# Performance work log

Hardware: AMD Instinct MI355X
Metric: run time of the kernel (lower is better)

Reference implementation:

```python
import jax, jax.numpy as jnp
import numpy as np

B, H, W, C = 8, 64, 64, 768
NH, HD = 12, 64          # num_heads, head_dim
WS = 16                  # window size
SCALE = HD ** -0.5


def setup_inputs() -> dict:
    key = jax.random.key(0)
    ks = jax.random.split(key, 6)
    x = jax.random.normal(ks[0], (B, H * W, C), dtype=jnp.float32)
    w_qkv = jax.random.normal(ks[1], (3 * C, C), dtype=jnp.float32) * 0.02
    w_out = jax.random.normal(ks[2], (C, C), dtype=jnp.float32) * 0.02
    b_out = jnp.zeros((C,), dtype=jnp.float32)
    rel_pos_h = jax.random.normal(ks[3], (2 * WS - 1, HD), dtype=jnp.float32) * 0.02
    rel_pos_w = jax.random.normal(ks[4], (2 * WS - 1, HD), dtype=jnp.float32) * 0.02
    return {"x": x, "w_qkv": w_qkv, "w_out": w_out, "b_out": b_out,
            "rel_pos_h": rel_pos_h, "rel_pos_w": rel_pos_w}


def reference(x, w_qkv, w_out, b_out, rel_pos_h, rel_pos_w):
    nh_w, nw_w = H // WS, W // WS
    xw = x.reshape(B, nh_w, WS, nw_w, WS, C).transpose(0, 1, 3, 2, 4, 5)
    Bw = B * nh_w * nw_w
    t = WS * WS
    xw = xw.reshape(Bw, t, C)

    # ---- qkv projection (no bias) and rearrange 'b t (qkv l d) -> qkv b l t d'
    qkv = (xw @ w_qkv.T).reshape(Bw, t, 3, NH, HD).transpose(2, 0, 3, 1, 4)
    q, k, v = qkv[0], qkv[1], qkv[2]        # each (Bw, NH, t, HD)

    # ---- scaled attention scores
    att = jnp.einsum('bhxd,bhyd->bhxy', q, k) * SCALE   # (Bw, NH, t, t)

    # ---- decomposed relative position bias (SAM/MViT style, q_size == k_size == WS)
    idx = jnp.arange(WS)[:, None] - jnp.arange(WS)[None, :] + (WS - 1)  # (WS, WS)
    Rh = rel_pos_h[idx]                      # (WS, WS, HD)
    Rw = rel_pos_w[idx]                      # (WS, WS, HD)
    rq = q.reshape(Bw * NH, WS, WS, HD)
    rel_h = jnp.einsum('bhwc,hkc->bhwk', rq, Rh)   # (Bw*NH, WS, WS, WS)
    rel_w = jnp.einsum('bhwc,wkc->bhwk', rq, Rw)
    att = (att.reshape(Bw * NH, WS, WS, WS, WS)
           + rel_h[:, :, :, :, None]
           + rel_w[:, :, :, None, :]).reshape(Bw, NH, t, t)

    # ---- softmax + AV
    att = jax.nn.softmax(att, axis=-1)
    o = jnp.einsum('bhxy,bhyd->bhxd', att, v)          # (Bw, NH, t, HD)
    o = o.transpose(0, 2, 1, 3).reshape(Bw, t, C)      # 'b h l d -> b l (h d)'

    # ---- output projection
    o = o @ w_out.T + b_out

    # ---- window unpartition back to (B, H*W, C)
    o = o.reshape(B, nh_w, nw_w, WS, WS, C).transpose(0, 1, 3, 2, 4, 5)
    return o.reshape(B, H * W, C)
```

## Files before the change

kernel.cpp:

```cpp
#include <hip/hip_runtime.h>

typedef __attribute__((ext_vector_type(8))) short bf16x8;
typedef __attribute__((ext_vector_type(4))) float f32x4;
typedef unsigned short u16;

__device__ __forceinline__ u16 f2bf(float f) {
  union { float f; unsigned u; } v; v.f = f;
  unsigned r = v.u + 0x7fffu + ((v.u >> 16) & 1u);
  return (u16)(r >> 16);
}
__device__ __forceinline__ float bf2f(u16 u) {
  union { unsigned u; float f; } v; v.u = ((unsigned)u) << 16;
  return v.f;
}
__device__ __forceinline__ void gload16(const void* g, void* l) {
  __builtin_amdgcn_global_load_lds((const __attribute__((address_space(1))) void*)g,
                                   (__attribute__((address_space(3))) void*)l, 16, 0, 0);
}

#define PH_BAR __builtin_amdgcn_s_barrier()
#define LGKM0  asm volatile("s_waitcnt lgkmcnt(0)" ::: "memory")
#define VM6    asm volatile("s_waitcnt vmcnt(6)" ::: "memory")
#define VM0    asm volatile("s_waitcnt vmcnt(0)" ::: "memory")

__global__ void sab_cvt_kernel(const float* __restrict__ src, u16* __restrict__ dst, int n4) {
  int i = blockIdx.x * blockDim.x + threadIdx.x;
  if (i >= n4) return;
  float4 f = reinterpret_cast<const float4*>(src)[i];
  ushort4 o; o.x = f2bf(f.x); o.y = f2bf(f.y); o.z = f2bf(f.z); o.w = f2bf(f.w);
  reinterpret_cast<ushort4*>(dst)[i] = o;
}

__global__ void sab_xw_kernel(const float* __restrict__ x, u16* __restrict__ xw) {
  const int total = 32768 * 192;
  for (int idx = blockIdx.x * 256 + threadIdx.x; idx < total; idx += gridDim.x * 256) {
    const int r = idx / 192, c = idx - r * 192;
    const int w = r >> 8, tt = r & 255;
    const long xrow = (long)(w >> 4) * 4096 + (((w >> 2) & 3) * 16 + (tt >> 4)) * 64 + (w & 3) * 16 + (tt & 15);
    float4 f = reinterpret_cast<const float4*>(x)[xrow * 192 + c];
    ushort4 o; o.x = f2bf(f.x); o.y = f2bf(f.y); o.z = f2bf(f.z); o.w = f2bf(f.w);
    reinterpret_cast<ushort4*>(xw)[idx] = o;
  }
}

template<int EPI>
__global__ __launch_bounds__(512, 2)
void sab_gemm8_kernel(const u16* __restrict__ A, const u16* __restrict__ Bt,
                      u16* __restrict__ outB, u16* __restrict__ vTp,
                      float* __restrict__ outF, const float* __restrict__ bias,
                      const int K)
{
  __shared__ __align__(16) u16 lds[2][2][2][8192];
  const int tid = threadIdx.x;
  const int lane = tid & 63, wid = tid >> 6;
  const int wr = wid >> 2, wc = wid & 3;
  const int lr = lane & 15, lg = lane >> 4;

  const int NY = gridDim.y;
  const int bid0 = blockIdx.y * gridDim.x + blockIdx.x;
  const int xcd = bid0 & 7, local = bid0 >> 3;
  const long m0 = (long)(xcd * 16 + local / NY) * 256;
  const long n0 = (long)(local % NY) * 256;

  const int swz = ((lane & 7) ^ (lane >> 3)) << 3;
  const u16* Agl = A  + (m0 + wid * 8 + (lane >> 3)) * (long)K + swz;
  const u16* Bgl = Bt + (n0 + wid * 8 + (lane >> 3)) * (long)K + swz;

  f32x4 acc[8][4];
#pragma unroll
  for (int a = 0; a < 8; ++a)
#pragma unroll
    for (int b = 0; b < 4; ++b) acc[a][b] = (f32x4){0.f, 0.f, 0.f, 0.f};

  auto stage = [&](int buf, int mat, int half, int rb, int kt) {
    const u16* g = (mat ? Bgl : Agl) + (half * 128 + rb) * (long)K + kt;
    gload16(g, &lds[buf][mat][half][(rb + wid * 8) * 64]);
  };
  auto rdA4 = [&](int buf, int q, bf16x8 (&out)[4][2]) {
#pragma unroll
    for (int m2 = 0; m2 < 4; ++m2)
#pragma unroll
      for (int kc = 0; kc < 2; ++kc)
        out[m2][kc] = *reinterpret_cast<const bf16x8*>(
          &lds[buf][0][wr][(q * 64 + m2 * 16 + lr) * 64 + ((kc * 32 + lg * 8) ^ ((lr & 7) << 3))]);
  };
  auto rdB2 = [&](int buf, int q, bf16x8 (&out)[2][2]) {
#pragma unroll
    for (int n2 = 0; n2 < 2; ++n2)
#pragma unroll
      for (int kc = 0; kc < 2; ++kc)
        out[n2][kc] = *reinterpret_cast<const bf16x8*>(
          &lds[buf][1][wc >> 1][((wc & 1) * 64 + q * 32 + n2 * 16 + lr) * 64 + ((kc * 32 + lg * 8) ^ ((lr & 7) << 3))]);
  };
  auto mma16 = [&](bf16x8 (&a)[4][2], bf16x8 (&b)[2][2], int mq, int nq) {
    __builtin_amdgcn_s_setprio(1);
#pragma unroll
    for (int kc = 0; kc < 2; ++kc)
#pragma unroll
      for (int m2 = 0; m2 < 4; ++m2)
#pragma unroll
        for (int n2 = 0; n2 < 2; ++n2)
          acc[mq * 4 + m2][nq * 2 + n2] = __builtin_amdgcn_mfma_f32_16x16x32_bf16(
              a[m2][kc], b[n2][kc], acc[mq * 4 + m2][nq * 2 + n2], 0, 0, 0);
    __builtin_amdgcn_s_setprio(0);
  };

  stage(0,0,0,0,0);  stage(0,0,1,0,0);  stage(0,1,0,0,0);  stage(0,1,1,0,0);
  stage(0,1,0,64,0); stage(0,1,1,64,0); stage(0,0,0,64,0); stage(0,0,1,64,0);
  stage(1,0,0,0,64); stage(1,0,1,0,64); stage(1,1,0,0,64); stage(1,1,1,0,64);
  stage(1,1,0,64,64); stage(1,1,1,64,64);
  VM6; PH_BAR;

  bf16x8 af[4][2], b0[2][2], b1[2][2];

  for (int kt = 0; kt < K; kt += 128) {
    const int k2 = kt + 128, k3 = kt + 192;
    const bool s2 = k2 < K, s3 = k3 < K;
    rdA4(0, 0, af); rdB2(0, 0, b0);
    stage(1,0,0,64, kt + 64); stage(1,0,1,64, kt + 64);
    PH_BAR; LGKM0; mma16(af, b0, 0, 0); PH_BAR;
    rdB2(0, 1, b1);
    if (s2) { stage(0,0,0,0, k2); stage(0,0,1,0, k2); }
    PH_BAR; LGKM0; mma16(af, b1, 0, 1); PH_BAR;
    rdA4(0, 1, af);
    if (s2) { stage(0,1,0,0, k2); stage(0,1,1,0, k2); }
    PH_BAR; LGKM0; mma16(af, b0, 1, 0); PH_BAR;
    if (s2) { stage(0,1,0,64, k2); stage(0,1,1,64, k2); }
    PH_BAR; mma16(af, b1, 1, 1); VM6; PH_BAR;
    rdA4(1, 0, af); rdB2(1, 0, b0);
    if (s2) { stage(0,0,0,64, k2); stage(0,0,1,64, k2); }
    PH_BAR; LGKM0; mma16(af, b0, 0, 0); PH_BAR;
    rdB2(1, 1, b1);
    if (s3) { stage(1,0,0,0, k3); stage(1,0,1,0, k3); }
    PH_BAR; LGKM0; mma16(af, b1, 0, 1); PH_BAR;
    rdA4(1, 1, af);
    if (s3) { stage(1,1,0,0, k3); stage(1,1,1,0, k3); }
    PH_BAR; LGKM0; mma16(af, b0, 1, 0); PH_BAR;
    if (s3) { stage(1,1,0,64, k3); stage(1,1,1,64, k3); }
    PH_BAR; mma16(af, b1, 1, 1); VM6; PH_BAR;
  }

  VM0;
  __syncthreads();
  u16* cl = &lds[0][0][0][0];

  if (EPI == 0) {
    if (n0 < 1536) {
#pragma unroll
      for (int mt = 0; mt < 8; ++mt)
#pragma unroll
        for (int nt = 0; nt < 4; ++nt) {
          const int col = wc * 64 + nt * 16 + lr;
          const int row0 = wr * 128 + mt * 16 + lg * 4;
#pragma unroll
          for (int r = 0; r < 4; ++r)
            cl[(row0 + r) * 256 + col] = f2bf(acc[mt][nt][r]);
        }
      __syncthreads();
#pragma unroll
      for (int s = 0; s < 16; ++s) {
        const int c = s * 512 + tid;
        const int row = c >> 5, ch = c & 31;
        *reinterpret_cast<bf16x8*>(&outB[(m0 + row) * 1536 + n0 + ch * 8]) =
            *reinterpret_cast<const bf16x8*>(&cl[row * 256 + ch * 8]);
      }
    } else {
#pragma unroll
      for (int mt = 0; mt < 8; ++mt)
#pragma unroll
        for (int nt = 0; nt < 4; ++nt) {
          const int col = wc * 64 + nt * 16 + lr;
          const int row0 = wr * 128 + mt * 16 + lg * 4;
          ushort4 o;
          o.x = f2bf(acc[mt][nt][0]); o.y = f2bf(acc[mt][nt][1]);
          o.z = f2bf(acc[mt][nt][2]); o.w = f2bf(acc[mt][nt][3]);
          *reinterpret_cast<ushort4*>(&cl[col * 256 + row0]) = o;
        }
      __syncthreads();
#pragma unroll
      for (int s = 0; s < 16; ++s) {
        const int c = s * 512 + tid;
        const int d = c >> 5, ch = c & 31;
        *reinterpret_cast<bf16x8*>(&vTp[(n0 - 1536 + d) * 32768L + m0 + ch * 8]) =
            *reinterpret_cast<const bf16x8*>(&cl[d * 256 + ch * 8]);
      }
    }
  } else {
#pragma unroll
    for (int mt = 0; mt < 8; ++mt)
#pragma unroll
      for (int nt = 0; nt < 4; ++nt) {
        const long col = n0 + wc * 64 + nt * 16 + lr;
        const float bv = bias[col];
        const long row0 = m0 + wr * 128 + mt * 16 + lg * 4;
#pragma unroll
        for (int r = 0; r < 4; ++r) {
          const int rr = (int)(row0 + r);
          const int w = rr >> 8, tt = rr & 255;
          const long xrow = (long)(w >> 4) * 4096 + (((w >> 2) & 3) * 16 + (tt >> 4)) * 64 + (w & 3) * 16 + (tt & 15);
          outF[xrow * 768 + col] = acc[mt][nt][r] + bv;
        }
      }
  }
}

__global__ __launch_bounds__(256, 2)
void sab_attn_kernel(const u16* __restrict__ qk, const u16* __restrict__ vT,
                     const float* __restrict__ rph, const float* __restrict__ rpw,
                     u16* __restrict__ oatt)
{
  __shared__ __align__(16) u16 relh_s[256 * 16];
  __shared__ __align__(16) u16 relw_s[256 * 16];
  __shared__ __align__(16) u16 Sbuf[4][16 * 72];

  const int blk0 = blockIdx.x;
  const int blk = (blk0 & 7) * 192 + (blk0 >> 3);
  const int w = blk / 12, h = blk % 12;
  const long qbase = (long)w * 256;
  const int tid = threadIdx.x, lane = tid & 63, wid = tid >> 6;
  const int lr = lane & 15, lg = lane >> 4;

  const u16* Qp = qk + (long)h * 64;
  const u16* Kp = qk + 768 + (long)h * 64;
  const u16* Vt = vT + (long)h * 64 * 32768 + w * 256;

#pragma unroll
  for (int ii = 0; ii < 4; ++ii) {
    const int i = wid * 4 + ii;
    f32x4 acc = (f32x4){0.f, 0.f, 0.f, 0.f};
#pragma unroll
    for (int kc = 0; kc < 2; ++kc) {
      bf16x8 a = *reinterpret_cast<const bf16x8*>(&Qp[(qbase + i * 16 + lr) * 1536 + kc * 32 + lg * 8]);
      const float* bp = rph + (i - lr + 15) * 64 + kc * 32 + lg * 8;
      bf16x8 b;
#pragma unroll
      for (int e = 0; e < 8; ++e) b[e] = (short)f2bf(bp[e]);
      acc = __builtin_amdgcn_mfma_f32_16x16x32_bf16(a, b, acc, 0, 0, 0);
    }
#pragma unroll
    for (int r = 0; r < 4; ++r)
      relh_s[(i * 16 + lg * 4 + r) * 16 + lr] = f2bf(acc[r]);
  }
#pragma unroll
  for (int jj = 0; jj < 4; ++jj) {
    const int j = wid * 4 + jj;
    f32x4 acc = (f32x4){0.f, 0.f, 0.f, 0.f};
#pragma unroll
    for (int kc = 0; kc < 2; ++kc) {
      bf16x8 a = *reinterpret_cast<const bf16x8*>(&Qp[(qbase + lr * 16 + j) * 1536 + kc * 32 + lg * 8]);
      const float* bp = rpw + (j - lr + 15) * 64 + kc * 32 + lg * 8;
      bf16x8 b;
#pragma unroll
      for (int e = 0; e < 8; ++e) b[e] = (short)f2bf(bp[e]);
      acc = __builtin_amdgcn_mfma_f32_16x16x32_bf16(a, b, acc, 0, 0, 0);
    }
#pragma unroll
    for (int r = 0; r < 4; ++r)
      relw_s[((lg * 4 + r) * 16 + j) * 16 + lr] = f2bf(acc[r]);
  }
  __syncthreads();

  bf16x8 qa[4][2];
#pragma unroll
  for (int mt = 0; mt < 4; ++mt)
#pragma unroll
    for (int kc = 0; kc < 2; ++kc)
      qa[mt][kc] = *reinterpret_cast<const bf16x8*>(&Qp[(qbase + wid * 64 + mt * 16 + lr) * 1536 + kc * 32 + lg * 8]);

  float rw[4][4];
#pragma unroll
  for (int mt = 0; mt < 4; ++mt)
#pragma unroll
    for (int r = 0; r < 4; ++r)
      rw[mt][r] = bf2f(relw_s[(wid * 64 + mt * 16 + lg * 4 + r) * 16 + lr]);

  float mrun[4][4], lrun[4][4];
  f32x4 oacc[4][4];
#pragma unroll
  for (int mt = 0; mt < 4; ++mt)
#pragma unroll
    for (int r = 0; r < 4; ++r) { mrun[mt][r] = -1e30f; lrun[mt][r] = 0.f; }
#pragma unroll
  for (int mt = 0; mt < 4; ++mt)
#pragma unroll
    for (int nt = 0; nt < 4; ++nt) oacc[mt][nt] = (f32x4){0.f, 0.f, 0.f, 0.f};

  u16* sb = &Sbuf[wid][0];

  for (int kb = 0; kb < 4; ++kb) {
    bf16x8 kf[4][2], vf[4][2];
#pragma unroll
    for (int nt = 0; nt < 4; ++nt)
#pragma unroll
      for (int kc = 0; kc < 2; ++kc) {
        kf[nt][kc] = *reinterpret_cast<const bf16x8*>(&Kp[(qbase + kb * 64 + nt * 16 + lr) * 1536 + kc * 32 + lg * 8]);
        vf[nt][kc] = *reinterpret_cast<const bf16x8*>(&Vt[(nt * 16 + lr) * 32768L + kb * 64 + kc * 32 + lg * 8]);
      }

#pragma unroll
    for (int mt = 0; mt < 4; ++mt) {
      f32x4 sn[4];
#pragma unroll
      for (int nt = 0; nt < 4; ++nt) {
        f32x4 t = (f32x4){0.f, 0.f, 0.f, 0.f};
#pragma unroll
        for (int kc = 0; kc < 2; ++kc)
          t = __builtin_amdgcn_mfma_f32_16x16x32_bf16(qa[mt][kc], kf[nt][kc], t, 0, 0, 0);
        sn[nt] = t;
      }
#pragma unroll
      for (int r = 0; r < 4; ++r) {
        const int x = wid * 64 + mt * 16 + lg * 4 + r;
        float sv[4];
#pragma unroll
        for (int nt = 0; nt < 4; ++nt)
          sv[nt] = sn[nt][r] * 0.125f + bf2f(relh_s[x * 16 + kb * 4 + nt]) + rw[mt][r];
        float rmax = fmaxf(fmaxf(sv[0], sv[1]), fmaxf(sv[2], sv[3]));
        rmax = fmaxf(rmax, __shfl_xor(rmax, 1));
        rmax = fmaxf(rmax, __shfl_xor(rmax, 2));
        rmax = fmaxf(rmax, __shfl_xor(rmax, 4));
        rmax = fmaxf(rmax, __shfl_xor(rmax, 8));
        const float mnew = fmaxf(mrun[mt][r], rmax);
        const float sf = __expf(mrun[mt][r] - mnew);
        mrun[mt][r] = mnew;
        float rsum = 0.f;
#pragma unroll
        for (int nt = 0; nt < 4; ++nt) { const float p = __expf(sv[nt] - mnew); sv[nt] = p; rsum += p; }
        lrun[mt][r] = lrun[mt][r] * sf + rsum;
#pragma unroll
        for (int nt = 0; nt < 4; ++nt) oacc[mt][nt][r] *= sf;
        const int rowl = lg * 4 + r;
#pragma unroll
        for (int nt = 0; nt < 4; ++nt) sb[rowl * 72 + nt * 16 + lr] = f2bf(sv[nt]);
      }
#pragma unroll
      for (int kc = 0; kc < 2; ++kc) {
        bf16x8 pa = *reinterpret_cast<const bf16x8*>(&sb[lr * 72 + kc * 32 + lg * 8]);
#pragma unroll
        for (int nt = 0; nt < 4; ++nt)
          oacc[mt][nt] = __builtin_amdgcn_mfma_f32_16x16x32_bf16(pa, vf[nt][kc], oacc[mt][nt], 0, 0, 0);
      }
    }
  }

#pragma unroll
  for (int mt = 0; mt < 4; ++mt)
#pragma unroll
    for (int r = 0; r < 4; ++r) {
      float lt = lrun[mt][r];
      lt += __shfl_xor(lt, 1);
      lt += __shfl_xor(lt, 2);
      lt += __shfl_xor(lt, 4);
      lt += __shfl_xor(lt, 8);
      const float inv = 1.f / lt;
      const long row = qbase + wid * 64 + mt * 16 + lg * 4 + r;
#pragma unroll
      for (int nt = 0; nt < 4; ++nt)
        oatt[row * 768 + h * 64 + nt * 16 + lr] = f2bf(oacc[mt][nt][r] * inv);
    }
}

extern "C" void kernel_launch(void* const* d_in, const int* in_sizes, int n_in,
                              void* d_out, int out_size, void* d_ws, size_t ws_size,
                              hipStream_t stream) {
  (void)in_sizes; (void)n_in; (void)out_size; (void)ws_size;
  const float* x     = (const float*)d_in[0];
  const float* w_qkv = (const float*)d_in[1];
  const float* w_out = (const float*)d_in[2];
  const float* b_out = (const float*)d_in[3];
  const float* rph   = (const float*)d_in[4];
  const float* rpw   = (const float*)d_in[5];
  float* out = (float*)d_out;

  char* ws = (char*)d_ws;
  u16* qk    = (u16*)ws;
  u16* vT    = (u16*)(ws + 100663296L);
  u16* xw    = (u16*)(ws + 150994944L);
  u16* wqkvb = (u16*)(ws + 201326592L);
  u16* woutb = (u16*)(ws + 204865536L);
  u16* oatt  = xw;

  sab_cvt_kernel<<<dim3(1728), dim3(256), 0, stream>>>(w_qkv, wqkvb, 442368);
  sab_cvt_kernel<<<dim3(576), dim3(256), 0, stream>>>(w_out, woutb, 147456);
  sab_xw_kernel<<<dim3(6144), dim3(256), 0, stream>>>(x, xw);
  sab_gemm8_kernel<0><<<dim3(128, 9), dim3(512), 0, stream>>>(xw, wqkvb, qk, vT, nullptr, nullptr, 768);
  sab_attn_kernel<<<dim3(1536), dim3(256), 0, stream>>>(qk, vT, rph, rpw, oatt);
  sab_gemm8_kernel<1><<<dim3(128, 3), dim3(512), 0, stream>>>(oatt, woutb, nullptr, nullptr, out, b_out, 768);
}
```

Measured before the change: 356.7 us.

## Use 16 waves per GEMM block with 2x8 warp grid and halved per-wave tiles

The 256x256-tile bf16 GEMM now runs with 1024 threads (16 waves) instead of 512, arranged 2x8 so each wave owns a 128x32 sub-tile. Staging is rebalanced so each wave issues half as many global-to-LDS loads, and the vmcnt waits change to match. The epilogues are adjusted for the narrower per-wave columns. This cuts per-wave accumulator registers and loads and adds waves for latency hiding, but each wave re-reads the A fragments from LDS with less reuse per B fragment, and fewer blocks fit per CU.

```diff
diff --git a/kernel.cpp b/kernel.cpp
--- a/kernel.cpp
+++ b/kernel.cpp
@@ -20,7 +20,7 @@
 
 #define PH_BAR __builtin_amdgcn_s_barrier()
 #define LGKM0  asm volatile("s_waitcnt lgkmcnt(0)" ::: "memory")
-#define VM6    asm volatile("s_waitcnt vmcnt(6)" ::: "memory")
+#define VM3    asm volatile("s_waitcnt vmcnt(3)" ::: "memory")
 #define VM0    asm volatile("s_waitcnt vmcnt(0)" ::: "memory")
 
 __global__ void sab_cvt_kernel(const float* __restrict__ src, u16* __restrict__ dst, int n4) {
@@ -44,7 +44,7 @@
 }
 
 template<int EPI>
-__global__ __launch_bounds__(512, 2)
+__global__ __launch_bounds__(1024)
 void sab_gemm8_kernel(const u16* __restrict__ A, const u16* __restrict__ Bt,
                       u16* __restrict__ outB, u16* __restrict__ vTp,
                       float* __restrict__ outF, const float* __restrict__ bias,
@@ -53,7 +53,7 @@
   __shared__ __align__(16) u16 lds[2][2][2][8192];
   const int tid = threadIdx.x;
   const int lane = tid & 63, wid = tid >> 6;
-  const int wr = wid >> 2, wc = wid & 3;
+  const int wr = wid >> 3, wc = wid & 7;
   const int lr = lane & 15, lg = lane >> 4;
 
   const int NY = gridDim.y;
@@ -62,19 +62,21 @@
   const long m0 = (long)(xcd * 16 + local / NY) * 256;
   const long n0 = (long)(local % NY) * 256;
 
-  const int swz = ((lane & 7) ^ (lane >> 3)) << 3;
-  const u16* Agl = A  + (m0 + wid * 8 + (lane >> 3)) * (long)K + swz;
-  const u16* Bgl = Bt + (n0 + wid * 8 + (lane >> 3)) * (long)K + swz;
-
-  f32x4 acc[8][4];
+  const int shalf = wid >> 3;
+  const int srow  = (wid & 7) * 8 + (lane >> 3);
+  const int swz   = ((lane & 7) ^ ((lane >> 3) & 7)) << 3;
+  const u16* Agl = A  + (m0 + shalf * 128 + srow) * (long)K + swz;
+  const u16* Bgl = Bt + (n0 + shalf * 128 + srow) * (long)K + swz;
+
+  f32x4 acc[8][2];
 #pragma unroll
   for (int a = 0; a < 8; ++a)
 #pragma unroll
-    for (int b = 0; b < 4; ++b) acc[a][b] = (f32x4){0.f, 0.f, 0.f, 0.f};
-
-  auto stage = [&](int buf, int mat, int half, int rb, int kt) {
-    const u16* g = (mat ? Bgl : Agl) + (half * 128 + rb) * (long)K + kt;
-    gload16(g, &lds[buf][mat][half][(rb + wid * 8) * 64]);
+    for (int b = 0; b < 2; ++b) acc[a][b] = (f32x4){0.f, 0.f, 0.f, 0.f};
+
+  auto stage = [&](int buf, int mat, int q, int kt) {
+    const u16* g = (mat ? Bgl : Agl) + (long)q * 64 * K + kt;
+    gload16(g, &lds[buf][mat][shalf][(q * 64 + (wid & 7) * 8) * 64]);
   };
   auto rdA4 = [&](int buf, int q, bf16x8 (&out)[4][2]) {
 #pragma unroll
@@ -84,60 +86,56 @@
         out[m2][kc] = *reinterpret_cast<const bf16x8*>(
           &lds[buf][0][wr][(q * 64 + m2 * 16 + lr) * 64 + ((kc * 32 + lg * 8) ^ ((lr & 7) << 3))]);
   };
-  auto rdB2 = [&](int buf, int q, bf16x8 (&out)[2][2]) {
-#pragma unroll
-    for (int n2 = 0; n2 < 2; ++n2)
-#pragma unroll
-      for (int kc = 0; kc < 2; ++kc)
-        out[n2][kc] = *reinterpret_cast<const bf16x8*>(
-          &lds[buf][1][wc >> 1][((wc & 1) * 64 + q * 32 + n2 * 16 + lr) * 64 + ((kc * 32 + lg * 8) ^ ((lr & 7) << 3))]);
+  auto rdB1 = [&](int buf, int nq, bf16x8 (&out)[2]) {
+#pragma unroll
+    for (int kc = 0; kc < 2; ++kc)
+      out[kc] = *reinterpret_cast<const bf16x8*>(
+        &lds[buf][1][wc >> 2][(((wc & 3) * 32 + nq * 16 + lr)) * 64 + ((kc * 32 + lg * 8) ^ ((lr & 7) << 3))]);
   };
-  auto mma16 = [&](bf16x8 (&a)[4][2], bf16x8 (&b)[2][2], int mq, int nq) {
+  auto mma8 = [&](bf16x8 (&a)[4][2], bf16x8 (&b)[2], int mq, int nq) {
     __builtin_amdgcn_s_setprio(1);
 #pragma unroll
     for (int kc = 0; kc < 2; ++kc)
 #pragma unroll
       for (int m2 = 0; m2 < 4; ++m2)
-#pragma unroll
-        for (int n2 = 0; n2 < 2; ++n2)
-          acc[mq * 4 + m2][nq * 2 + n2] = __builtin_amdgcn_mfma_f32_16x16x32_bf16(
-              a[m2][kc], b[n2][kc], acc[mq * 4 + m2][nq * 2 + n2], 0, 0, 0);
+        acc[mq * 4 + m2][nq] = __builtin_amdgcn_mfma_f32_16x16x32_bf16(
+            a[m2][kc], b[kc], acc[mq * 4 + m2][nq], 0, 0, 0);
     __builtin_amdgcn_s_setprio(0);
   };
 
-  stage(0,0,0,0,0);  stage(0,0,1,0,0);  stage(0,1,0,0,0);  stage(0,1,1,0,0);
-  stage(0,1,0,64,0); stage(0,1,1,64,0); stage(0,0,0,64,0); stage(0,0,1,64,0);
-  stage(1,0,0,0,64); stage(1,0,1,0,64); stage(1,1,0,0,64); stage(1,1,1,0,64);
-  stage(1,1,0,64,64); stage(1,1,1,64,64);
-  VM6; PH_BAR;
-
-  bf16x8 af[4][2], b0[2][2], b1[2][2];
+  stage(0,0,0,0); stage(0,0,1,0); stage(0,1,0,0); stage(0,1,1,0);
+  stage(1,0,0,64); stage(1,1,0,64); stage(1,1,1,64);
+  VM3; PH_BAR;
+
+  bf16x8 af[4][2], b0[2], b1[2];
 
   for (int kt = 0; kt < K; kt += 128) {
     const int k2 = kt + 128, k3 = kt + 192;
     const bool s2 = k2 < K, s3 = k3 < K;
-    rdA4(0, 0, af); rdB2(0, 0, b0);
-    stage(1,0,0,64, kt + 64); stage(1,0,1,64, kt + 64);
-    PH_BAR; LGKM0; mma16(af, b0, 0, 0); PH_BAR;
-    rdB2(0, 1, b1);
-    if (s2) { stage(0,0,0,0, k2); stage(0,0,1,0, k2); }
-    PH_BAR; LGKM0; mma16(af, b1, 0, 1); PH_BAR;
+    rdA4(0, 0, af); rdB1(0, 0, b0);
+    stage(1,0,1, kt + 64);
+    PH_BAR; LGKM0; mma8(af, b0, 0, 0); PH_BAR;
+    rdB1(0, 1, b1);
+    if (s2) stage(0,0,0, k2);
+    PH_BAR; LGKM0; mma8(af, b1, 0, 1); PH_BAR;
     rdA4(0, 1, af);
-    if (s2) { stage(0,1,0,0, k2); stage(0,1,1,0, k2); }
-    PH_BAR; LGKM0; mma16(af, b0, 1, 0); PH_BAR;
-    if (s2) { stage(0,1,0,64, k2); stage(0,1,1,64, k2); }
-    PH_BAR; mma16(af, b1, 1, 1); VM6; PH_BAR;
-    rdA4(1, 0, af); rdB2(1, 0, b0);
-    if (s2) { stage(0,0,0,64, k2); stage(0,0,1,64, k2); }
-    PH_BAR; LGKM0; mma16(af, b0, 0, 0); PH_BAR;
-    rdB2(1, 1, b1);
-    if (s3) { stage(1,0,0,0, k3); stage(1,0,1,0, k3); }
-    PH_BAR; LGKM0; mma16(af, b1, 0, 1); PH_BAR;
+    if (s2) stage(0,1,0, k2);
+    PH_BAR; LGKM0; mma8(af, b0, 1, 0); PH_BAR;
+    if (s2) stage(0,1,1, k2);
+    PH_BAR; mma8(af, b1, 1, 1);
+    if (s2) { VM3; } else { VM0; }
+    PH_BAR;
+    rdA4(1, 0, af); rdB1(1, 0, b0);
+    if (s2) stage(0,0,1, k2);
+    PH_BAR; LGKM0; mma8(af, b0, 0, 0); PH_BAR;
+    rdB1(1, 1, b1);
+    if (s3) stage(1,0,0, k3);
+    PH_BAR; LGKM0; mma8(af, b1, 0, 1); PH_BAR;
     rdA4(1, 1, af);
-    if (s3) { stage(1,1,0,0, k3); stage(1,1,1,0, k3); }
-    PH_BAR; LGKM0; mma16(af, b0, 1, 0); PH_BAR;
-    if (s3) { stage(1,1,0,64, k3); stage(1,1,1,64, k3); }
-    PH_BAR; mma16(af, b1, 1, 1); VM6; PH_BAR;
+    if (s3) stage(1,1,0, k3);
+    PH_BAR; LGKM0; mma8(af, b0, 1, 0); PH_BAR;
+    if (s3) stage(1,1,1, k3);
+    PH_BAR; mma8(af, b1, 1, 1); VM3; PH_BAR;
   }
 
   VM0;
@@ -149,8 +147,8 @@
 #pragma unroll
       for (int mt = 0; mt < 8; ++mt)
 #pragma unroll
-        for (int nt = 0; nt < 4; ++nt) {
-          const int col = wc * 64 + nt * 16 + lr;
+        for (int nt = 0; nt < 2; ++nt) {
+          const int col = wc * 32 + nt * 16 + lr;
           const int row0 = wr * 128 + mt * 16 + lg * 4;
 #pragma unroll
           for (int r = 0; r < 4; ++r)
@@ -158,8 +156,8 @@
         }
       __syncthreads();
 #pragma unroll
-      for (int s = 0; s < 16; ++s) {
-        const int c = s * 512 + tid;
+      for (int s = 0; s < 8; ++s) {
+        const int c = s * 1024 + tid;
         const int row = c >> 5, ch = c & 31;
         *reinterpret_cast<bf16x8*>(&outB[(m0 + row) * 1536 + n0 + ch * 8]) =
             *reinterpret_cast<const bf16x8*>(&cl[row * 256 + ch * 8]);
@@ -168,8 +166,8 @@
 #pragma unroll
       for (int mt = 0; mt < 8; ++mt)
 #pragma unroll
-        for (int nt = 0; nt < 4; ++nt) {
-          const int col = wc * 64 + nt * 16 + lr;
+        for (int nt = 0; nt < 2; ++nt) {
+          const int col = wc * 32 + nt * 16 + lr;
           const int row0 = wr * 128 + mt * 16 + lg * 4;
           ushort4 o;
           o.x = f2bf(acc[mt][nt][0]); o.y = f2bf(acc[mt][nt][1]);
@@ -178,8 +176,8 @@
         }
       __syncthreads();
 #pragma unroll
-      for (int s = 0; s < 16; ++s) {
-        const int c = s * 512 + tid;
+      for (int s = 0; s < 8; ++s) {
+        const int c = s * 1024 + tid;
         const int d = c >> 5, ch = c & 31;
         *reinterpret_cast<bf16x8*>(&vTp[(n0 - 1536 + d) * 32768L + m0 + ch * 8]) =
             *reinterpret_cast<const bf16x8*>(&cl[d * 256 + ch * 8]);
@@ -189,8 +187,8 @@
 #pragma unroll
     for (int mt = 0; mt < 8; ++mt)
 #pragma unroll
-      for (int nt = 0; nt < 4; ++nt) {
-        const long col = n0 + wc * 64 + nt * 16 + lr;
+      for (int nt = 0; nt < 2; ++nt) {
+        const long col = n0 + wc * 32 + nt * 16 + lr;
         const float bv = bias[col];
         const long row0 = m0 + wr * 128 + mt * 16 + lg * 4;
 #pragma unroll
@@ -383,7 +381,7 @@
   sab_cvt_kernel<<<dim3(1728), dim3(256), 0, stream>>>(w_qkv, wqkvb, 442368);
   sab_cvt_kernel<<<dim3(576), dim3(256), 0, stream>>>(w_out, woutb, 147456);
   sab_xw_kernel<<<dim3(6144), dim3(256), 0, stream>>>(x, xw);
-  sab_gemm8_kernel<0><<<dim3(128, 9), dim3(512), 0, stream>>>(xw, wqkvb, qk, vT, nullptr, nullptr, 768);
+  sab_gemm8_kernel<0><<<dim3(128, 9), dim3(1024), 0, stream>>>(xw, wqkvb, qk, vT, nullptr, nullptr, 768);
   sab_attn_kernel<<<dim3(1536), dim3(256), 0, stream>>>(qk, vT, rph, rpw, oatt);
-  sab_gemm8_kernel<1><<<dim3(128, 3), dim3(512), 0, stream>>>(oatt, woutb, nullptr, nullptr, out, b_out, 768);
-}
+  sab_gemm8_kernel<1><<<dim3(128, 3), dim3(1024), 0, stream>>>(oatt, woutb, nullptr, nullptr, out, b_out, 768);
+}
```

After: 611.4 us. 1.71x slower.
